# Optimization experiments

Hardware: AMD Instinct MI355X
Metric: run time of the kernel (lower is better)

Reference implementation:

```python
import jax, jax.numpy as jnp
import numpy as np
from itertools import product

B, D, H, W = 2, 32, 256, 256
N = 150000
C_IN, C_MID, C_OUT = 16, 32, 64
STRIDE, PAD, K = 2, 1, 3
DO = (D + 2 * PAD - K) // STRIDE + 1
HO = (H + 2 * PAD - K) // STRIDE + 1
WO = (W + 2 * PAD - K) // STRIDE + 1
EPS = 1e-5


def setup_inputs() -> dict:
    key = jax.random.key(0)
    ks = jax.random.split(key, 8)
    # unique active voxel coords via permutation of linear grid indices
    lin = jax.random.permutation(ks[0], B * D * H * W)[:N]
    b = lin // (D * H * W); r = lin % (D * H * W)
    z = r // (H * W); r = r % (H * W)
    y = r // W; x = r % W
    coords = jnp.stack([b, z, y, x], axis=1).astype(jnp.int32)  # [N,4] = (batch,z,y,x)
    feats = jax.random.normal(ks[1], (N, C_IN), jnp.float32)
    W1 = jax.random.normal(ks[2], (27, C_IN, C_MID), jnp.float32) * 0.08
    W2 = jax.random.normal(ks[3], (27, C_MID, C_MID), jnp.float32) * 0.06
    W3 = jax.random.normal(ks[4], (27, C_MID, C_OUT), jnp.float32) * 0.06
    b1 = jnp.zeros((C_MID,), jnp.float32); g1 = jnp.ones((C_MID,), jnp.float32); be1 = jnp.zeros((C_MID,), jnp.float32)
    b2 = jnp.zeros((C_MID,), jnp.float32); g2 = jnp.ones((C_MID,), jnp.float32); be2 = jnp.zeros((C_MID,), jnp.float32)
    b3 = jnp.zeros((C_OUT,), jnp.float32); g3 = jnp.ones((C_OUT,), jnp.float32); be3 = jnp.zeros((C_OUT,), jnp.float32)
    return dict(feats=feats, coords=coords, W1=W1, b1=b1, g1=g1, be1=be1,
                W2=W2, b2=b2, g2=g2, be2=be2, W3=W3, b3=b3, g3=g3, be3=be3)


def _bn_relu(x, g, b):
    # BatchNorm1d (training batch stats, biased var) over active voxels + ReLU
    m = x.mean(0)
    v = ((x - m) ** 2).mean(0)
    return jax.nn.relu((x - m) * jax.lax.rsqrt(v + EPS) * g + b)


def _subm_conv(feats, coords, grid, Wk, bias):
    # submanifold conv: gather neighbor features per kernel offset, GEMM, accumulate
    bb, zz, yy, xx = coords[:, 0], coords[:, 1], coords[:, 2], coords[:, 3]
    acc = jnp.zeros((feats.shape[0], Wk.shape[-1]), feats.dtype)
    for ki, (dz, dy, dx) in enumerate(product((-1, 0, 1), repeat=3)):
        nz, ny, nx = zz + dz, yy + dy, xx + dx
        valid = (nz >= 0) & (nz < D) & (ny >= 0) & (ny < H) & (nx >= 0) & (nx < W)
        lin = ((bb * D + jnp.clip(nz, 0, D - 1)) * H + jnp.clip(ny, 0, H - 1)) * W + jnp.clip(nx, 0, W - 1)
        nidx = jnp.where(valid, grid[lin], -1)
        gathered = jnp.where((nidx >= 0)[:, None], feats[jnp.maximum(nidx, 0)], 0.0)
        acc = acc + gathered @ Wk[ki]
    return acc + bias


def _sparse_down_conv(feats, coords, Wk, bias):
    # stride-2 SparseConv3d as GEMM + scatter-add into downsampled dense grid; mask = active outputs
    bb, zz, yy, xx = coords[:, 0], coords[:, 1], coords[:, 2], coords[:, 3]
    M = B * DO * HO * WO
    out = jnp.zeros((M, Wk.shape[-1]), feats.dtype)
    cnt = jnp.zeros((M,), jnp.int32)
    for ki, (kz, ky, kx) in enumerate(product(range(K), repeat=3)):
        oz, oy, ox = zz + PAD - kz, yy + PAD - ky, xx + PAD - kx
        valid = ((oz % STRIDE == 0) & (oy % STRIDE == 0) & (ox % STRIDE == 0) &
                 (oz >= 0) & (oy >= 0) & (ox >= 0) &
                 (oz // STRIDE < DO) & (oy // STRIDE < HO) & (ox // STRIDE < WO))
        lin = ((bb * DO + jnp.clip(oz // STRIDE, 0, DO - 1)) * HO
               + jnp.clip(oy // STRIDE, 0, HO - 1)) * WO + jnp.clip(ox // STRIDE, 0, WO - 1)
        lin = jnp.where(valid, lin, 0)
        contrib = jnp.where(valid[:, None], feats @ Wk[ki], 0.0)
        out = out.at[lin].add(contrib)
        cnt = cnt.at[lin].add(valid.astype(jnp.int32))
    mask = cnt > 0
    out = jnp.where(mask[:, None], out + bias, 0.0)
    return out, mask


def reference(feats, coords, W1, b1, g1, be1, W2, b2, g2, be2, W3, b3, g3, be3):
    lin0 = ((coords[:, 0] * D + coords[:, 1]) * H + coords[:, 2]) * W + coords[:, 3]
    grid = jnp.full((B * D * H * W,), -1, jnp.int32).at[lin0].set(jnp.arange(N, dtype=jnp.int32))
    x = _bn_relu(_subm_conv(feats, coords, grid, W1, b1), g1, be1)
    x = _bn_relu(_subm_conv(x, coords, grid, W2, b2), g2, be2)
    out, mask = _sparse_down_conv(x, coords, W3, b3)
    nact = jnp.maximum(mask.sum(), 1).astype(out.dtype)
    m = out.sum(0) / nact  # inactive rows are zero
    v = jnp.where(mask[:, None], (out - m) ** 2, 0.0).sum(0) / nact
    out = jax.nn.relu((out - m) * jax.lax.rsqrt(v + EPS) * g3 + be3)
    out = jnp.where(mask[:, None], out, 0.0)
    return out.reshape(B, DO, HO, WO, C_OUT)
```

## Files before the change

### kernel.cpp

```cpp
#include <hip/hip_runtime.h>

#define B_   2
#define D_   32
#define H_   256
#define W_   256
#define N_   150000
#define CIN  16
#define CMID 32
#define COUT 64
#define DO_  16
#define HO_  128
#define WO_  128
#define M_   (B_*DO_*HO_*WO_)
#define EPSf 1e-5f
#define NB_DOWN 8192
#define NREP 64

typedef _Float16 h2 __attribute__((ext_vector_type(2)));
__device__ inline h2 as_h2(unsigned u) { union { unsigned u; h2 h; } x; x.u = u; return x.h; }

#if defined(__has_builtin) && __has_builtin(__builtin_amdgcn_fdot2)
__device__ inline float dot2(unsigned f, unsigned w, float acc) {
    return __builtin_amdgcn_fdot2(as_h2(f), as_h2(w), acc, false);
}
#else
__device__ inline float dot2(unsigned f, unsigned w, float acc) {
    const h2 a = as_h2(f), b = as_h2(w);
    return fmaf((float)a.x, (float)b.x, fmaf((float)a.y, (float)b.y, acc));
}
#endif

__device__ inline unsigned hpk(float a, float b) {
    union { _Float16 h[2]; unsigned u; } x;
    x.h[0] = (_Float16)a; x.h[1] = (_Float16)b; return x.u;
}

__global__ __launch_bounds__(256) void k_scatter(const int* __restrict__ coords,
                                                 int* __restrict__ grid) {
    int i = blockIdx.x * 256 + threadIdx.x;
    if (i >= N_) return;
    const int4 c = *(const int4*)(coords + 4 * (size_t)i);
    grid[((c.x * D_ + c.y) * H_ + c.z) * W_ + c.w] = i;
}

__global__ __launch_bounds__(256) void k_twisth(const float* __restrict__ W1,
                                                const float* __restrict__ W2,
                                                const float* __restrict__ W3,
                                                uint4* __restrict__ Wh1,
                                                uint4* __restrict__ Wh2,
                                                uint4* __restrict__ Wh3) {
    const int t = blockIdx.x * 256 + threadIdx.x;
    if (t < 1728) {
        const int ki = t / 64, r = t % 64, half = r >> 5, sub = r & 31;
        const float* base = W1 + ki * 512 + (half * 8) * 32 + sub;
        uint4 o;
        o.x = hpk(base[0],   base[32]);
        o.y = hpk(base[64],  base[96]);
        o.z = hpk(base[128], base[160]);
        o.w = hpk(base[192], base[224]);
        Wh1[(ki * 2 + half) * 32 + sub] = o;
    } else if (t < 1728 + 3456) {
        const int u = t - 1728;
        const int ki = u / 128, r = u % 128, qh = r >> 5, sub = r & 31;
        const int half = qh >> 1, q = qh & 1;
        const float* base = W2 + ki * 1024 + (half * 16 + q * 8) * 32 + sub;
        uint4 o;
        o.x = hpk(base[0],   base[32]);
        o.y = hpk(base[64],  base[96]);
        o.z = hpk(base[128], base[160]);
        o.w = hpk(base[192], base[224]);
        Wh2[((ki * 2 + half) * 2 + q) * 32 + sub] = o;
    } else if (t < 1728 + 3456 + 6912) {
        const int u = t - 5184;
        const int ki = u / 256, r = u % 256, q = r >> 6, lane = r & 63;
        const float* base = W3 + ki * 2048 + (q * 8) * 64 + lane;
        uint4 o;
        o.x = hpk(base[0],   base[64]);
        o.y = hpk(base[128], base[192]);
        o.z = hpk(base[256], base[320]);
        o.w = hpk(base[384], base[448]);
        Wh3[(ki * 4 + q) * 64 + lane] = o;
    }
}

__global__ __launch_bounds__(256) void k_feat16(const float* __restrict__ F,
                                                unsigned* __restrict__ F16) {
    const int i = blockIdx.x * 256 + threadIdx.x;
    if (i >= N_ * CIN / 4) return;
    const float4 v = ((const float4*)F)[i];
    uint2 o; o.x = hpk(v.x, v.y); o.y = hpk(v.z, v.w);
    ((uint2*)F16)[i] = o;
}

template <int CI>
__global__ __launch_bounds__(256) void k_subm(const unsigned* __restrict__ X16,
                                              const int* __restrict__ coords,
                                              const int* __restrict__ grid,
                                              const uint4* __restrict__ Wh,
                                              const float* __restrict__ bias,
                                              _Float16* __restrict__ Yp,
                                              float* __restrict__ slab0) {
    constexpr int NQ = CI / 16;
    const int wid  = (blockIdx.x * 256 + threadIdx.x) >> 6;
    const int lane = threadIdx.x & 63;
    const int sub  = lane & 31;
    const int half = lane >> 5;
    const int i0   = wid * 4;

    int nidx01 = -1, nidx23 = -1;
    {
        const int4 cc = *(const int4*)(coords + 4 * (size_t)(i0 + half));
        if (sub < 27) {
            const int nz = cc.y + sub / 9 - 1;
            const int ny = cc.z + (sub / 3) % 3 - 1;
            const int nx = cc.w + sub % 3 - 1;
            if ((unsigned)nz < (unsigned)D_ && (unsigned)ny < (unsigned)H_ &&
                (unsigned)nx < (unsigned)W_)
                nidx01 = grid[((cc.x * D_ + nz) * H_ + ny) * W_ + nx];
        }
    }
    {
        const int4 cc = *(const int4*)(coords + 4 * (size_t)(i0 + 2 + half));
        if (sub < 27) {
            const int nz = cc.y + sub / 9 - 1;
            const int ny = cc.z + (sub / 3) % 3 - 1;
            const int nx = cc.w + sub % 3 - 1;
            if ((unsigned)nz < (unsigned)D_ && (unsigned)ny < (unsigned)H_ &&
                (unsigned)nx < (unsigned)W_)
                nidx23 = grid[((cc.x * D_ + nz) * H_ + ny) * W_ + nx];
        }
    }
    const unsigned long long a01 = __ballot(nidx01 >= 0);
    const unsigned long long a23 = __ballot(nidx23 >= 0);
    unsigned m0 = (unsigned)a01 & 0x7FFFFFFu;
    unsigned m1 = (unsigned)(a01 >> 32) & 0x7FFFFFFu;
    unsigned m2 = (unsigned)a23 & 0x7FFFFFFu;
    unsigned m3 = (unsigned)(a23 >> 32) & 0x7FFFFFFu;

    float4 ac0 = {0.f, 0.f, 0.f, 0.f}, ac1 = {0.f, 0.f, 0.f, 0.f};
    float4 ac2 = {0.f, 0.f, 0.f, 0.f}, ac3 = {0.f, 0.f, 0.f, 0.f};

    auto tap = [&](int ki, int ni, float4& ac) {
        const uint4* __restrict__ f =
            (const uint4*)(X16 + (size_t)ni * (CI / 2) + half * (CI / 4));
        const uint4* __restrict__ wb = Wh + ((size_t)(ki * 2 + half)) * NQ * 32 + sub;
#pragma unroll
        for (int q = 0; q < NQ; ++q) {
            const uint4 fu = f[q];
            const uint4 wu = wb[q * 32];
            ac.x = dot2(fu.x, wu.x, ac.x);
            ac.y = dot2(fu.y, wu.y, ac.y);
            ac.z = dot2(fu.z, wu.z, ac.z);
            ac.w = dot2(fu.w, wu.w, ac.w);
        }
    };

    while (m0 | m1 | m2 | m3) {
        if (m0) { const int ki = __builtin_ctz(m0); m0 &= m0 - 1;
                  tap(ki, __shfl(nidx01, ki, 64),      ac0); }
        if (m1) { const int ki = __builtin_ctz(m1); m1 &= m1 - 1;
                  tap(ki, __shfl(nidx01, ki + 32, 64), ac1); }
        if (m2) { const int ki = __builtin_ctz(m2); m2 &= m2 - 1;
                  tap(ki, __shfl(nidx23, ki, 64),      ac2); }
        if (m3) { const int ki = __builtin_ctz(m3); m3 &= m3 - 1;
                  tap(ki, __shfl(nidx23, ki + 32, 64), ac3); }
    }

    float s0 = (ac0.x + ac0.y) + (ac0.z + ac0.w);
    float s1 = (ac1.x + ac1.y) + (ac1.z + ac1.w);
    float s2v = (ac2.x + ac2.y) + (ac2.z + ac2.w);
    float s3 = (ac3.x + ac3.y) + (ac3.z + ac3.w);
    s0 += __shfl_xor(s0, 32, 64);
    s1 += __shfl_xor(s1, 32, 64);
    s2v += __shfl_xor(s2v, 32, 64);
    s3 += __shfl_xor(s3, 32, 64);
    const float bv  = bias[sub];
    const float o01 = (half ? s1 : s0) + bv;
    const float o23 = (half ? s3 : s2v) + bv;
    Yp[(size_t)(i0 + half) * 32 + sub]     = (_Float16)o01;
    Yp[(size_t)(i0 + 2 + half) * 32 + sub] = (_Float16)o23;

    __shared__ float sd[256];
    const int tid = threadIdx.x;
    float* __restrict__ slab = slab0 + (size_t)(blockIdx.x & (NREP - 1)) * 64;
    sd[tid] = o01 + o23;
    __syncthreads();
    if (tid < 32) {
        float t = 0.f;
#pragma unroll
        for (int k = 0; k < 8; ++k) t += sd[tid + 32 * k];
        atomicAdd(slab + tid, t);
    }
    __syncthreads();
    sd[tid] = o01 * o01 + o23 * o23;
    __syncthreads();
    if (tid < 32) {
        float t = 0.f;
#pragma unroll
        for (int k = 0; k < 8; ++k) t += sd[tid + 32 * k];
        atomicAdd(slab + 32 + tid, t);
    }
}

__global__ __launch_bounds__(256) void k_down(const unsigned* __restrict__ X16,
                                              const int* __restrict__ grid,
                                              const uint4* __restrict__ Wh3,
                                              const float* __restrict__ bias,
                                              _Float16* __restrict__ Yh,
                                              unsigned char* __restrict__ mask,
                                              float* __restrict__ slab0,
                                              int* __restrict__ nacts) {
    const int b    = blockIdx.x;
    const int swz  = (b & 7) * (NB_DOWN / 8) + (b >> 3);
    const int tid  = threadIdx.x;
    const int wv   = tid >> 6;
    const int lane = tid & 63;
    const int sub  = lane & 31;
    const int half = lane >> 5;

    const int vox0 = swz * 64;
    const int ox0  = vox0 & 127;
    int t = vox0 >> 7;
    const int oy = t & 127; t >>= 7;
    const int oz = t & 15;
    const int bb = t >> 4;

    __shared__ int   gl[9][132];
    __shared__ float sd[256];
    __shared__ int   scnt[4];

    const int gx0 = 2 * ox0 - 1;
#pragma unroll
    for (int r = 0; r < 9; ++r) {
        const int z = 2 * oz - 1 + r / 3;
        const int y = 2 * oy - 1 + r % 3;
        if (tid < 132) {
            const int xo = tid;
            const int x  = gx0 + xo;
            int v = -1;
            if ((unsigned)z < (unsigned)D_ && (unsigned)y < (unsigned)H_ &&
                (unsigned)x < (unsigned)W_ && xo < 129)
                v = grid[((bb * D_ + z) * H_ + y) * W_ + x];
            gl[r][xo] = v;
        }
    }
    __syncthreads();

    const int dz = sub / 9, dy = (sub / 3) % 3, dx = sub % 3;
    const int row = (sub < 27) ? dz * 3 + dy : 0;

    const float bv = bias[lane];
    float s = 0.f, s2 = 0.f;
    int cnt = 0;

    auto tap = [&](int ki, int ni, float4& ac) {
        const uint4* __restrict__ fS = (const uint4*)(X16 + (size_t)ni * 16);
        const uint4* __restrict__ wb = Wh3 + (size_t)ki * 256 + lane;
#pragma unroll
        for (int q = 0; q < 4; ++q) {
            const uint4 fu = fS[q];
            const uint4 wu = wb[q * 64];
            ac.x = dot2(fu.x, wu.x, ac.x);
            ac.y = dot2(fu.y, wu.y, ac.y);
            ac.z = dot2(fu.z, wu.z, ac.z);
            ac.w = dot2(fu.w, wu.w, ac.w);
        }
    };

    int n01 = (sub < 27) ? gl[row][2 * (wv * 16 + half) + dx] : -1;
    int n23 = (sub < 27) ? gl[row][2 * (wv * 16 + 2 + half) + dx] : -1;

    for (int it = 0; it < 4; ++it) {
        const int v0  = wv * 16 + it * 4;
        const int c01 = n01, c23 = n23;
        const unsigned long long a01 = __ballot(c01 >= 0);
        const unsigned long long a23 = __ballot(c23 >= 0);

        if (it < 3) {
            n01 = (sub < 27) ? gl[row][2 * (v0 + 4 + half) + dx] : -1;
            n23 = (sub < 27) ? gl[row][2 * (v0 + 6 + half) + dx] : -1;
        }

        unsigned m0 = (unsigned)a01 & 0x7FFFFFFu;
        unsigned m1 = (unsigned)(a01 >> 32) & 0x7FFFFFFu;
        unsigned m2 = (unsigned)a23 & 0x7FFFFFFu;
        unsigned m3 = (unsigned)(a23 >> 32) & 0x7FFFFFFu;
        const int mk0 = m0 ? 1 : 0, mk1 = m1 ? 1 : 0;
        const int mk2 = m2 ? 1 : 0, mk3 = m3 ? 1 : 0;

        float4 ac0 = {0.f, 0.f, 0.f, 0.f}, ac1 = {0.f, 0.f, 0.f, 0.f};
        float4 ac2 = {0.f, 0.f, 0.f, 0.f}, ac3 = {0.f, 0.f, 0.f, 0.f};
        while (m0 | m1 | m2 | m3) {
            if (m0) { const int ki = __builtin_ctz(m0); m0 &= m0 - 1;
                      tap(ki, __builtin_amdgcn_readfirstlane(__shfl(c01, ki, 64)),      ac0); }
            if (m1) { const int ki = __builtin_ctz(m1); m1 &= m1 - 1;
                      tap(ki, __builtin_amdgcn_readfirstlane(__shfl(c01, ki + 32, 64)), ac1); }
            if (m2) { const int ki = __builtin_ctz(m2); m2 &= m2 - 1;
                      tap(ki, __builtin_amdgcn_readfirstlane(__shfl(c23, ki, 64)),      ac2); }
            if (m3) { const int ki = __builtin_ctz(m3); m3 &= m3 - 1;
                      tap(ki, __builtin_amdgcn_readfirstlane(__shfl(c23, ki + 32, 64)), ac3); }
        }

        const int vg = vox0 + v0;
        const float o0 = mk0 ? (ac0.x + ac0.y) + (ac0.z + ac0.w) + bv : 0.f;
        const float o1 = mk1 ? (ac1.x + ac1.y) + (ac1.z + ac1.w) + bv : 0.f;
        const float o2 = mk2 ? (ac2.x + ac2.y) + (ac2.z + ac2.w) + bv : 0.f;
        const float o3 = mk3 ? (ac3.x + ac3.y) + (ac3.z + ac3.w) + bv : 0.f;
        Yh[(size_t)vg * COUT + lane]       = (_Float16)o0;
        Yh[(size_t)(vg + 1) * COUT + lane] = (_Float16)o1;
        Yh[(size_t)(vg + 2) * COUT + lane] = (_Float16)o2;
        Yh[(size_t)(vg + 3) * COUT + lane] = (_Float16)o3;
        if (lane == 0) {
            mask[vg]     = (unsigned char)mk0;
            mask[vg + 1] = (unsigned char)mk1;
            mask[vg + 2] = (unsigned char)mk2;
            mask[vg + 3] = (unsigned char)mk3;
            cnt += mk0 + mk1 + mk2 + mk3;
        }
        s  += o0 + o1 + o2 + o3;
        s2 += o0 * o0 + o1 * o1 + o2 * o2 + o3 * o3;
    }

    float* __restrict__ slab = slab0 + (size_t)(b & (NREP - 1)) * 128;
    sd[tid] = s;
    if (lane == 0) scnt[wv] = cnt;
    __syncthreads();
    if (tid < 64) atomicAdd(slab + tid, sd[tid] + sd[tid + 64] + sd[tid + 128] + sd[tid + 192]);
    __syncthreads();
    sd[tid] = s2;
    __syncthreads();
    if (tid < 64) atomicAdd(slab + 64 + tid, sd[tid] + sd[tid + 64] + sd[tid + 128] + sd[tid + 192]);
    if (tid == 0) atomicAdd(nacts + (b & (NREP - 1)), scnt[0] + scnt[1] + scnt[2] + scnt[3]);
}

template <int C>
__global__ void k_finslab(const float* __restrict__ slab0,
                          const float* __restrict__ g,
                          const float* __restrict__ be,
                          float n, float* __restrict__ ss) {
    const int c = threadIdx.x;
    if (c >= C) return;
    float sm = 0.f, s2 = 0.f;
    for (int r = 0; r < NREP; ++r) {
        sm += slab0[r * 2 * C + c];
        s2 += slab0[r * 2 * C + C + c];
    }
    const float m  = sm / n;
    const float v  = s2 / n - m * m;
    const float sc = g[c] * rsqrtf(v + EPSf);
    ss[c]     = sc;
    ss[C + c] = be[c] - m * sc;
}

__global__ void k_finstats3(const float* __restrict__ slab0,
                            const int* __restrict__ nacts,
                            const float* __restrict__ g,
                            const float* __restrict__ be,
                            float* __restrict__ ss) {
    const int c = threadIdx.x;
    if (c >= 64) return;
    float sm = 0.f, s2 = 0.f;
    int na = 0;
    for (int r = 0; r < NREP; ++r) {
        sm += slab0[r * 128 + c];
        s2 += slab0[r * 128 + 64 + c];
        na += nacts[r];
    }
    const float n  = (float)(na > 0 ? na : 1);
    const float m  = sm / n;
    const float v  = s2 / n - m * m;
    const float sc = g[c] * rsqrtf(v + EPSf);
    ss[c]      = sc;
    ss[64 + c] = be[c] - m * sc;
}

template <int C>
__global__ __launch_bounds__(256) void k_norm16(const unsigned* __restrict__ Yp2,
                                                const float* __restrict__ ss,
                                                unsigned* __restrict__ Xo16, long n4) {
    const long t = (long)blockIdx.x * 256 + threadIdx.x;
    if (t >= n4) return;
    const uint2 y = ((const uint2*)Yp2)[t];
    const h2 lo = as_h2(y.x), hi = as_h2(y.y);
    const int ch = (int)((t * 4) % C);
    float ox = fmaxf(fmaf((float)lo.x, ss[ch],     ss[C + ch]),     0.f);
    float oy = fmaxf(fmaf((float)lo.y, ss[ch + 1], ss[C + ch + 1]), 0.f);
    float oz = fmaxf(fmaf((float)hi.x, ss[ch + 2], ss[C + ch + 2]), 0.f);
    float ow = fmaxf(fmaf((float)hi.y, ss[ch + 3], ss[C + ch + 3]), 0.f);
    uint2 o; o.x = hpk(ox, oy); o.y = hpk(oz, ow);
    ((uint2*)Xo16)[t] = o;
}

__global__ __launch_bounds__(256) void k_norm3(const _Float16* __restrict__ Yh,
                                               const unsigned char* __restrict__ mask,
                                               const float* __restrict__ ss,
                                               float* __restrict__ out) {
    const long n4 = (long)M_ * COUT / 4;
    const long t = (long)blockIdx.x * 256 + threadIdx.x;
    if (t >= n4) return;
    const long vox = t >> 4;
    const int ch = (int)((t * 4) & 63);
    float4 o;
    if (mask[vox]) {
        const uint2 yu = *(const uint2*)(Yh + t * 4);
        const h2 ylo = as_h2(yu.x), yhi = as_h2(yu.y);
        o.x = fmaxf(fmaf((float)ylo.x, ss[ch],     ss[64 + ch]),     0.f);
        o.y = fmaxf(fmaf((float)ylo.y, ss[ch + 1], ss[64 + ch + 1]), 0.f);
        o.z = fmaxf(fmaf((float)yhi.x, ss[ch + 2], ss[64 + ch + 2]), 0.f);
        o.w = fmaxf(fmaf((float)yhi.y, ss[ch + 3], ss[64 + ch + 3]), 0.f);
    } else {
        o.x = o.y = o.z = o.w = 0.f;
    }
    ((float4*)out)[t] = o;
}

extern "C" void kernel_launch(void* const* d_in, const int* in_sizes, int n_in,
                              void* d_out, int out_size, void* d_ws, size_t ws_size,
                              hipStream_t stream) {
    const float* feats = (const float*)d_in[0];
    const int*   coords = (const int*)d_in[1];
    const float* W1 = (const float*)d_in[2];
    const float* b1 = (const float*)d_in[3];
    const float* g1 = (const float*)d_in[4];
    const float* be1 = (const float*)d_in[5];
    const float* W2 = (const float*)d_in[6];
    const float* b2 = (const float*)d_in[7];
    const float* g2 = (const float*)d_in[8];
    const float* be2 = (const float*)d_in[9];
    const float* W3 = (const float*)d_in[10];
    const float* b3 = (const float*)d_in[11];
    const float* g3 = (const float*)d_in[12];
    const float* be3 = (const float*)d_in[13];
    float* out = (float*)d_out;

    char* ws = (char*)d_ws;
    const size_t gridBytes = (size_t)B_ * D_ * H_ * W_ * 4;
    const size_t f16Bytes  = (size_t)N_ * CIN * 2;
    const size_t bufPBytes = (size_t)N_ * CMID * 2;
    const size_t YhBytes   = (size_t)M_ * COUT * 2;
    int*       grid   = (int*)ws;
    unsigned*  feat16 = (unsigned*)(ws + gridBytes);
    _Float16*  bufP   = (_Float16*)(ws + gridBytes + f16Bytes);
    unsigned*  bufH   = (unsigned*)(ws + gridBytes + f16Bytes + bufPBytes);
    _Float16*  Yh     = (_Float16*)(ws + gridBytes + f16Bytes + 2 * bufPBytes);
    unsigned char* mask = (unsigned char*)(ws + gridBytes + f16Bytes + 2 * bufPBytes + YhBytes);
    float* stats = (float*)(ws + gridBytes + f16Bytes + 2 * bufPBytes + YhBytes + (size_t)M_);

    float* ss1   = stats;
    float* ss2   = stats + 64;
    float* ss3   = stats + 128;
    float* slab1 = stats + 1024;
    float* slab2 = stats + 1024 + NREP * 64;
    float* slab3 = stats + 1024 + NREP * 128;
    int*   nacts = (int*)(stats + 1024 + NREP * 256);
    uint4* Wh1 = (uint4*)(stats + 32768);
    uint4* Wh2 = Wh1 + 1728;
    uint4* Wh3 = Wh2 + 3456;

    hipMemsetAsync(grid, 0xFF, gridBytes, stream);
    hipMemsetAsync(stats + 1024, 0, (NREP * 256 + NREP) * 4, stream);

    k_scatter<<<(N_ + 255) / 256, 256, 0, stream>>>(coords, grid);
    k_twisth<<<(12096 + 255) / 256, 256, 0, stream>>>(W1, W2, W3, Wh1, Wh2, Wh3);
    k_feat16<<<(N_ * CIN / 4 + 255) / 256, 256, 0, stream>>>(feats, feat16);

    const int nb_subm = N_ / 16;
    k_subm<CIN><<<nb_subm, 256, 0, stream>>>(feat16, coords, grid, Wh1, b1, bufP, slab1);
    k_finslab<CMID><<<1, 64, 0, stream>>>(slab1, g1, be1, (float)N_, ss1);
    k_norm16<CMID><<<(N_ * CMID / 4 + 255) / 256, 256, 0, stream>>>(
        (const unsigned*)bufP, ss1, bufH, (long)N_ * CMID / 4);

    k_subm<CMID><<<nb_subm, 256, 0, stream>>>(bufH, coords, grid, Wh2, b2, bufP, slab2);
    k_finslab<CMID><<<1, 64, 0, stream>>>(slab2, g2, be2, (float)N_, ss2);
    k_norm16<CMID><<<(N_ * CMID / 4 + 255) / 256, 256, 0, stream>>>(
        (const unsigned*)bufP, ss2, bufH, (long)N_ * CMID / 4);

    k_down<<<NB_DOWN, 256, 0, stream>>>(bufH, grid, Wh3, b3, Yh, mask, slab3, nacts);
    k_finstats3<<<1, 64, 0, stream>>>(slab3, nacts, g3, be3, ss3);
    k_norm3<<<(M_ * COUT / 4) / 256, 256, 0, stream>>>(Yh, mask, ss3, out);
}
```

Measured before the change: 240.4 us.

## Compact active taps per wave into a flat list and software-pipeline loads

In k_down, all active (voxel, kernel-offset) taps of a wave's 16 output voxels are now compacted into one lane-indexed list with ds_permute, together with metadata marking each voxel's last tap. The tap loop then walks this flat list four deep, issuing the feature and weight loads for the next taps before the current dot products, so memory latency overlaps compute. Before, the code looped per group of four voxels with ctz over the ballot masks, which left lanes idle when voxels had uneven tap counts. This costs more registers and more complex control flow, which may lower occupancy, and falls back to a serial per-voxel path when there are more than 62 taps.

```diff
diff --git a/kernel.cpp b/kernel.cpp
--- a/kernel.cpp
+++ b/kernel.cpp
@@ -28,6 +28,12 @@
     const h2 a = as_h2(f), b = as_h2(w);
     return fmaf((float)a.x, (float)b.x, fmaf((float)a.y, (float)b.y, acc));
 }
+#endif
+
+#if defined(__has_builtin) && __has_builtin(__builtin_amdgcn_readlane)
+#define RDLANE(v, l) __builtin_amdgcn_readlane((v), (l))
+#else
+#define RDLANE(v, l) __shfl((v), (l), 64)
 #endif
 
 __device__ inline unsigned hpk(float a, float b) {
@@ -220,10 +226,10 @@
 
     const int vox0 = swz * 64;
     const int ox0  = vox0 & 127;
-    int t = vox0 >> 7;
-    const int oy = t & 127; t >>= 7;
-    const int oz = t & 15;
-    const int bb = t >> 4;
+    int t0 = vox0 >> 7;
+    const int oy = t0 & 127; t0 >>= 7;
+    const int oz = t0 & 15;
+    const int bb = t0 >> 4;
 
     __shared__ int   gl[9][132];
     __shared__ float sd[256];
@@ -248,77 +254,142 @@
 
     const int dz = sub / 9, dy = (sub / 3) % 3, dx = sub % 3;
     const int row = (sub < 27) ? dz * 3 + dy : 0;
+    const int wbase = wv * 16;
+
+    int nP[8];
+    unsigned long long aP[8];
+#pragma unroll
+    for (int p = 0; p < 8; ++p) {
+        const int vl = wbase + 2 * p + half;
+        nP[p] = (sub < 27) ? gl[row][2 * vl + dx] : -1;
+        aP[p] = __ballot(nP[p] >= 0);
+    }
+
+    int pcA[16];
+#pragma unroll
+    for (int p = 0; p < 8; ++p) {
+        pcA[2 * p]     = __popcll(aP[p] & 0x7FFFFFFull);
+        pcA[2 * p + 1] = __popcll((aP[p] >> 32) & 0x7FFFFFFull);
+    }
+    int baseA[16]; int ntap = 0;
+#pragma unroll
+    for (int v = 0; v < 16; ++v) { baseA[v] = ntap; ntap += pcA[v]; }
 
     const float bv = bias[lane];
     float s = 0.f, s2 = 0.f;
     int cnt = 0;
 
-    auto tap = [&](int ki, int ni, float4& ac) {
-        const uint4* __restrict__ fS = (const uint4*)(X16 + (size_t)ni * 16);
-        const uint4* __restrict__ wb = Wh3 + (size_t)ki * 256 + lane;
-#pragma unroll
-        for (int q = 0; q < 4; ++q) {
-            const uint4 fu = fS[q];
-            const uint4 wu = wb[q * 64];
-            ac.x = dot2(fu.x, wu.x, ac.x);
-            ac.y = dot2(fu.y, wu.y, ac.y);
-            ac.z = dot2(fu.z, wu.z, ac.z);
-            ac.w = dot2(fu.w, wu.w, ac.w);
-        }
-    };
-
-    int n01 = (sub < 27) ? gl[row][2 * (wv * 16 + half) + dx] : -1;
-    int n23 = (sub < 27) ? gl[row][2 * (wv * 16 + 2 + half) + dx] : -1;
-
-    for (int it = 0; it < 4; ++it) {
-        const int v0  = wv * 16 + it * 4;
-        const int c01 = n01, c23 = n23;
-        const unsigned long long a01 = __ballot(c01 >= 0);
-        const unsigned long long a23 = __ballot(c23 >= 0);
-
-        if (it < 3) {
-            n01 = (sub < 27) ? gl[row][2 * (v0 + 4 + half) + dx] : -1;
-            n23 = (sub < 27) ? gl[row][2 * (v0 + 6 + half) + dx] : -1;
-        }
-
-        unsigned m0 = (unsigned)a01 & 0x7FFFFFFu;
-        unsigned m1 = (unsigned)(a01 >> 32) & 0x7FFFFFFu;
-        unsigned m2 = (unsigned)a23 & 0x7FFFFFFu;
-        unsigned m3 = (unsigned)(a23 >> 32) & 0x7FFFFFFu;
-        const int mk0 = m0 ? 1 : 0, mk1 = m1 ? 1 : 0;
-        const int mk2 = m2 ? 1 : 0, mk3 = m3 ? 1 : 0;
-
-        float4 ac0 = {0.f, 0.f, 0.f, 0.f}, ac1 = {0.f, 0.f, 0.f, 0.f};
-        float4 ac2 = {0.f, 0.f, 0.f, 0.f}, ac3 = {0.f, 0.f, 0.f, 0.f};
-        while (m0 | m1 | m2 | m3) {
-            if (m0) { const int ki = __builtin_ctz(m0); m0 &= m0 - 1;
-                      tap(ki, __builtin_amdgcn_readfirstlane(__shfl(c01, ki, 64)),      ac0); }
-            if (m1) { const int ki = __builtin_ctz(m1); m1 &= m1 - 1;
-                      tap(ki, __builtin_amdgcn_readfirstlane(__shfl(c01, ki + 32, 64)), ac1); }
-            if (m2) { const int ki = __builtin_ctz(m2); m2 &= m2 - 1;
-                      tap(ki, __builtin_amdgcn_readfirstlane(__shfl(c23, ki, 64)),      ac2); }
-            if (m3) { const int ki = __builtin_ctz(m3); m3 &= m3 - 1;
-                      tap(ki, __builtin_amdgcn_readfirstlane(__shfl(c23, ki + 32, 64)), ac3); }
-        }
-
-        const int vg = vox0 + v0;
-        const float o0 = mk0 ? (ac0.x + ac0.y) + (ac0.z + ac0.w) + bv : 0.f;
-        const float o1 = mk1 ? (ac1.x + ac1.y) + (ac1.z + ac1.w) + bv : 0.f;
-        const float o2 = mk2 ? (ac2.x + ac2.y) + (ac2.z + ac2.w) + bv : 0.f;
-        const float o3 = mk3 ? (ac3.x + ac3.y) + (ac3.z + ac3.w) + bv : 0.f;
-        Yh[(size_t)vg * COUT + lane]       = (_Float16)o0;
-        Yh[(size_t)(vg + 1) * COUT + lane] = (_Float16)o1;
-        Yh[(size_t)(vg + 2) * COUT + lane] = (_Float16)o2;
-        Yh[(size_t)(vg + 3) * COUT + lane] = (_Float16)o3;
+#pragma unroll
+    for (int v = 0; v < 16; ++v) {
+        if (pcA[v] == 0)
+            Yh[(size_t)(vox0 + wbase + v) * COUT + lane] = (_Float16)0.f;
         if (lane == 0) {
-            mask[vg]     = (unsigned char)mk0;
-            mask[vg + 1] = (unsigned char)mk1;
-            mask[vg + 2] = (unsigned char)mk2;
-            mask[vg + 3] = (unsigned char)mk3;
-            cnt += mk0 + mk1 + mk2 + mk3;
-        }
-        s  += o0 + o1 + o2 + o3;
-        s2 += o0 * o0 + o1 * o1 + o2 * o2 + o3 * o3;
+            const int a = pcA[v] ? 1 : 0;
+            mask[vox0 + wbase + v] = (unsigned char)a;
+            cnt += a;
+        }
+    }
+
+    if (ntap <= 62) {
+        int metaV = 0, niV = 0;
+#pragma unroll
+        for (int p = 0; p < 8; ++p) {
+            const unsigned mA = (unsigned)(aP[p] & 0x7FFFFFFull);
+            const unsigned mB = (unsigned)((aP[p] >> 32) & 0x7FFFFFFull);
+            const unsigned myM = half ? mB : mA;
+            const int  sb    = sub & 31;
+            const bool valid = (sub < 27) && ((myM >> sb) & 1u);
+            const unsigned below = myM & ((1u << sb) - 1u);
+            const int slot = (half ? baseA[2 * p + 1] : baseA[2 * p]) + __popc(below);
+            const int isLast = ((myM >> ((sb + 1) & 31)) == 0u) ? 1 : 0;
+            const int v = 2 * p + half;
+            const int meta = 0x8000 | (v << 5) | sb | (isLast << 9);
+            const int addr = (valid ? slot : 63) * 4;
+            metaV |= __builtin_amdgcn_ds_permute(addr, valid ? meta : 0);
+            niV   |= __builtin_amdgcn_ds_permute(addr, valid ? nP[p] : 0);
+        }
+
+        int zv = 0;
+        asm volatile("" : "+v"(zv));
+
+        float4 acc = {0.f, 0.f, 0.f, 0.f};
+
+        auto EXT = [&](int t, int& me, uint4* rf, uint4* rw) {
+            me = RDLANE(metaV, t);
+            const int ni = RDLANE(niV, t);
+            const uint4* fp = (const uint4*)(X16 + (size_t)(ni * 16 + zv));
+            const uint4* wp = Wh3 + (size_t)(me & 31) * 256 + lane;
+#pragma unroll
+            for (int q = 0; q < 4; ++q) { rf[q] = fp[q]; rw[q] = wp[q * 64]; }
+        };
+        auto CMP = [&](int me, const uint4* rf, const uint4* rw) {
+#pragma unroll
+            for (int q = 0; q < 4; ++q) {
+                acc.x = dot2(rf[q].x, rw[q].x, acc.x);
+                acc.y = dot2(rf[q].y, rw[q].y, acc.y);
+                acc.z = dot2(rf[q].z, rw[q].z, acc.z);
+                acc.w = dot2(rf[q].w, rw[q].w, acc.w);
+            }
+            if (me & 0x200) {
+                const int v = (me >> 5) & 15;
+                const float o = (acc.x + acc.y) + (acc.z + acc.w) + bv;
+                Yh[(size_t)(vox0 + wbase + v) * COUT + lane] = (_Float16)o;
+                s += o; s2 += o * o;
+                acc.x = 0.f; acc.y = 0.f; acc.z = 0.f; acc.w = 0.f;
+            }
+        };
+
+        uint4 rf0[4], rw0[4], rf1[4], rw1[4], rf2[4], rw2[4], rf3[4], rw3[4];
+        int me0 = 0, me1 = 0, me2 = 0, me3 = 0;
+        if (0 < ntap) EXT(0, me0, rf0, rw0);
+        if (1 < ntap) EXT(1, me1, rf1, rw1);
+        if (2 < ntap) EXT(2, me2, rf2, rw2);
+        if (3 < ntap) EXT(3, me3, rf3, rw3);
+        for (int t = 0; t < ntap; t += 4) {
+            CMP(me0, rf0, rw0);
+            if (t + 4 < ntap) EXT(t + 4, me0, rf0, rw0);
+            if (t + 1 < ntap) {
+                CMP(me1, rf1, rw1);
+                if (t + 5 < ntap) EXT(t + 5, me1, rf1, rw1);
+            }
+            if (t + 2 < ntap) {
+                CMP(me2, rf2, rw2);
+                if (t + 6 < ntap) EXT(t + 6, me2, rf2, rw2);
+            }
+            if (t + 3 < ntap) {
+                CMP(me3, rf3, rw3);
+                if (t + 7 < ntap) EXT(t + 7, me3, rf3, rw3);
+            }
+        }
+    } else {
+#pragma unroll
+        for (int v = 0; v < 16; ++v) {
+            const unsigned mv = (v & 1)
+                ? (unsigned)((aP[v >> 1] >> 32) & 0x7FFFFFFull)
+                : (unsigned)(aP[v >> 1] & 0x7FFFFFFull);
+            if (mv == 0) continue;
+            unsigned m = mv;
+            float acc1 = 0.f;
+            while (m) {
+                const int ki = __builtin_ctz(m); m &= m - 1;
+                const int ni = __builtin_amdgcn_readfirstlane(
+                                   __shfl(nP[v >> 1], ki + 32 * (v & 1), 64));
+                const uint4* __restrict__ fS = (const uint4*)(X16 + (size_t)ni * 16);
+                const uint4* __restrict__ wb = Wh3 + (size_t)ki * 256 + lane;
+#pragma unroll
+                for (int q = 0; q < 4; ++q) {
+                    const uint4 fu = fS[q];
+                    const uint4 wu = wb[q * 64];
+                    acc1 = dot2(fu.x, wu.x, acc1);
+                    acc1 = dot2(fu.y, wu.y, acc1);
+                    acc1 = dot2(fu.z, wu.z, acc1);
+                    acc1 = dot2(fu.w, wu.w, acc1);
+                }
+            }
+            const float o = acc1 + bv;
+            Yh[(size_t)(vox0 + wbase + v) * COUT + lane] = (_Float16)o;
+            s += o; s2 += o * o;
+        }
     }
 
     float* __restrict__ slab = slab0 + (size_t)(b & (NREP - 1)) * 128;
```

New measurement: 313.8 us. 1.31x slower.

## Rewrite strided downsample conv with MFMA 16x16x32 f16 matrix instructions

Applied to the files above, without the earlier changes.

The downsampling sparse conv kernel drops the sparse per-tap dot2 loop, which walked active neighbours via ballot and shuffle. Each wave now owns 16 output channels and runs a dense loop over all 27 taps, computing 16-voxel subtiles with MFMA f16 instructions. The weights are repacked into the MFMA operand layout, and subtiles are skipped only when no voxel in them has a neighbour at that tap. This trades sparse skipping for dense matrix throughput, so with very sparse inputs much of the MFMA work multiplies zeros. Each feature row is also gathered once per wave, four times per block.

```diff
diff --git a/kernel.cpp b/kernel.cpp
--- a/kernel.cpp
+++ b/kernel.cpp
@@ -17,6 +17,10 @@
 #define NREP 64
 
 typedef _Float16 h2 __attribute__((ext_vector_type(2)));
+typedef _Float16 v8h __attribute__((ext_vector_type(8)));
+typedef float    v4f __attribute__((ext_vector_type(4)));
+union U4H8 { uint4 u; v8h h; };
+
 __device__ inline h2 as_h2(unsigned u) { union { unsigned u; h2 h; } x; x.u = u; return x.h; }
 
 #if defined(__has_builtin) && __has_builtin(__builtin_amdgcn_fdot2)
@@ -48,7 +52,7 @@
                                                 const float* __restrict__ W3,
                                                 uint4* __restrict__ Wh1,
                                                 uint4* __restrict__ Wh2,
-                                                uint4* __restrict__ Wh3) {
+                                                uint4* __restrict__ Wm3) {
     const int t = blockIdx.x * 256 + threadIdx.x;
     if (t < 1728) {
         const int ki = t / 64, r = t % 64, half = r >> 5, sub = r & 31;
@@ -72,14 +76,19 @@
         Wh2[((ki * 2 + half) * 2 + q) * 32 + sub] = o;
     } else if (t < 1728 + 3456 + 6912) {
         const int u = t - 5184;
-        const int ki = u / 256, r = u % 256, q = r >> 6, lane = r & 63;
-        const float* base = W3 + ki * 2048 + (q * 8) * 64 + lane;
+        const int lane = u & 63;
+        const int rest = u >> 6;
+        const int w  = rest / 27;
+        const int ki = rest % 27;
+        const int k0 = (lane >> 4) * 8;
+        const int co = w * 16 + (lane & 15);
+        const float* base = W3 + ki * 2048 + co;
         uint4 o;
-        o.x = hpk(base[0],   base[64]);
-        o.y = hpk(base[128], base[192]);
-        o.z = hpk(base[256], base[320]);
-        o.w = hpk(base[384], base[448]);
-        Wh3[(ki * 4 + q) * 64 + lane] = o;
+        o.x = hpk(base[(k0 + 0) * 64], base[(k0 + 1) * 64]);
+        o.y = hpk(base[(k0 + 2) * 64], base[(k0 + 3) * 64]);
+        o.z = hpk(base[(k0 + 4) * 64], base[(k0 + 5) * 64]);
+        o.w = hpk(base[(k0 + 6) * 64], base[(k0 + 7) * 64]);
+        Wm3[u] = o;
     }
 }
 
@@ -204,7 +213,7 @@
 
 __global__ __launch_bounds__(256) void k_down(const unsigned* __restrict__ X16,
                                               const int* __restrict__ grid,
-                                              const uint4* __restrict__ Wh3,
+                                              const uint4* __restrict__ Wm3,
                                               const float* __restrict__ bias,
                                               _Float16* __restrict__ Yh,
                                               unsigned char* __restrict__ mask,
@@ -215,19 +224,18 @@
     const int tid  = threadIdx.x;
     const int wv   = tid >> 6;
     const int lane = tid & 63;
-    const int sub  = lane & 31;
-    const int half = lane >> 5;
+    const int col  = lane & 15;
+    const int kg   = lane >> 4;
 
     const int vox0 = swz * 64;
     const int ox0  = vox0 & 127;
-    int t = vox0 >> 7;
-    const int oy = t & 127; t >>= 7;
-    const int oz = t & 15;
-    const int bb = t >> 4;
+    int t0 = vox0 >> 7;
+    const int oy = t0 & 127; t0 >>= 7;
+    const int oz = t0 & 15;
+    const int bb = t0 >> 4;
 
     __shared__ int   gl[9][132];
     __shared__ float sd[256];
-    __shared__ int   scnt[4];
 
     const int gx0 = 2 * ox0 - 1;
 #pragma unroll
@@ -246,91 +254,73 @@
     }
     __syncthreads();
 
-    const int dz = sub / 9, dy = (sub / 3) % 3, dx = sub % 3;
-    const int row = (sub < 27) ? dz * 3 + dy : 0;
-
-    const float bv = bias[lane];
+    const float bias_l = bias[wv * 16 + col];
+    const uint4* __restrict__ wmrow = Wm3 + (size_t)(wv * 27) * 64 + lane;
+
+    v4f acc0 = {0.f, 0.f, 0.f, 0.f}, acc1 = {0.f, 0.f, 0.f, 0.f};
+    v4f acc2 = {0.f, 0.f, 0.f, 0.f}, acc3 = {0.f, 0.f, 0.f, 0.f};
+    unsigned any0 = 0, any1 = 0, any2 = 0, any3 = 0;
+
+    auto subtile = [&](int m, v4f& accv, unsigned& anyv, int row, int dxk, v8h wbh) {
+        const int ni = gl[row][2 * (16 * m + col) + dxk];
+        const unsigned long long blt = __ballot(ni >= 0);
+        if (blt) {
+            anyv |= (unsigned)blt & 0xFFFFu;
+            U4H8 af; af.u.x = 0u; af.u.y = 0u; af.u.z = 0u; af.u.w = 0u;
+            if (ni >= 0)
+                af.u = *(const uint4*)(X16 + (size_t)ni * 16 + kg * 4);
+            accv = __builtin_amdgcn_mfma_f32_16x16x32_f16(af.h, wbh, accv, 0, 0, 0);
+        }
+    };
+
+    for (int ki = 0; ki < 27; ++ki) {
+        const int row = ki / 3;
+        const int dxk = ki - row * 3;
+        U4H8 wb; wb.u = wmrow[ki * 64];
+        subtile(0, acc0, any0, row, dxk, wb.h);
+        subtile(1, acc1, any1, row, dxk, wb.h);
+        subtile(2, acc2, any2, row, dxk, wb.h);
+        subtile(3, acc3, any3, row, dxk, wb.h);
+    }
+
     float s = 0.f, s2 = 0.f;
-    int cnt = 0;
-
-    auto tap = [&](int ki, int ni, float4& ac) {
-        const uint4* __restrict__ fS = (const uint4*)(X16 + (size_t)ni * 16);
-        const uint4* __restrict__ wb = Wh3 + (size_t)ki * 256 + lane;
+    auto epi = [&](int m, const v4f& accv, unsigned anyv) {
 #pragma unroll
-        for (int q = 0; q < 4; ++q) {
-            const uint4 fu = fS[q];
-            const uint4 wu = wb[q * 64];
-            ac.x = dot2(fu.x, wu.x, ac.x);
-            ac.y = dot2(fu.y, wu.y, ac.y);
-            ac.z = dot2(fu.z, wu.z, ac.z);
-            ac.w = dot2(fu.w, wu.w, ac.w);
+        for (int r = 0; r < 4; ++r) {
+            const int rowloc = kg * 4 + r;
+            const float o = ((anyv >> rowloc) & 1u) ? (accv[r] + bias_l) : 0.f;
+            Yh[(size_t)(vox0 + 16 * m + rowloc) * COUT + wv * 16 + col] = (_Float16)o;
+            s += o; s2 += o * o;
         }
     };
-
-    int n01 = (sub < 27) ? gl[row][2 * (wv * 16 + half) + dx] : -1;
-    int n23 = (sub < 27) ? gl[row][2 * (wv * 16 + 2 + half) + dx] : -1;
-
-    for (int it = 0; it < 4; ++it) {
-        const int v0  = wv * 16 + it * 4;
-        const int c01 = n01, c23 = n23;
-        const unsigned long long a01 = __ballot(c01 >= 0);
-        const unsigned long long a23 = __ballot(c23 >= 0);
-
-        if (it < 3) {
-            n01 = (sub < 27) ? gl[row][2 * (v0 + 4 + half) + dx] : -1;
-            n23 = (sub < 27) ? gl[row][2 * (v0 + 6 + half) + dx] : -1;
-        }
-
-        unsigned m0 = (unsigned)a01 & 0x7FFFFFFu;
-        unsigned m1 = (unsigned)(a01 >> 32) & 0x7FFFFFFu;
-        unsigned m2 = (unsigned)a23 & 0x7FFFFFFu;
-        unsigned m3 = (unsigned)(a23 >> 32) & 0x7FFFFFFu;
-        const int mk0 = m0 ? 1 : 0, mk1 = m1 ? 1 : 0;
-        const int mk2 = m2 ? 1 : 0, mk3 = m3 ? 1 : 0;
-
-        float4 ac0 = {0.f, 0.f, 0.f, 0.f}, ac1 = {0.f, 0.f, 0.f, 0.f};
-        float4 ac2 = {0.f, 0.f, 0.f, 0.f}, ac3 = {0.f, 0.f, 0.f, 0.f};
-        while (m0 | m1 | m2 | m3) {
-            if (m0) { const int ki = __builtin_ctz(m0); m0 &= m0 - 1;
-                      tap(ki, __builtin_amdgcn_readfirstlane(__shfl(c01, ki, 64)),      ac0); }
-            if (m1) { const int ki = __builtin_ctz(m1); m1 &= m1 - 1;
-                      tap(ki, __builtin_amdgcn_readfirstlane(__shfl(c01, ki + 32, 64)), ac1); }
-            if (m2) { const int ki = __builtin_ctz(m2); m2 &= m2 - 1;
-                      tap(ki, __builtin_amdgcn_readfirstlane(__shfl(c23, ki, 64)),      ac2); }
-            if (m3) { const int ki = __builtin_ctz(m3); m3 &= m3 - 1;
-                      tap(ki, __builtin_amdgcn_readfirstlane(__shfl(c23, ki + 32, 64)), ac3); }
-        }
-
-        const int vg = vox0 + v0;
-        const float o0 = mk0 ? (ac0.x + ac0.y) + (ac0.z + ac0.w) + bv : 0.f;
-        const float o1 = mk1 ? (ac1.x + ac1.y) + (ac1.z + ac1.w) + bv : 0.f;
-        const float o2 = mk2 ? (ac2.x + ac2.y) + (ac2.z + ac2.w) + bv : 0.f;
-        const float o3 = mk3 ? (ac3.x + ac3.y) + (ac3.z + ac3.w) + bv : 0.f;
-        Yh[(size_t)vg * COUT + lane]       = (_Float16)o0;
-        Yh[(size_t)(vg + 1) * COUT + lane] = (_Float16)o1;
-        Yh[(size_t)(vg + 2) * COUT + lane] = (_Float16)o2;
-        Yh[(size_t)(vg + 3) * COUT + lane] = (_Float16)o3;
-        if (lane == 0) {
-            mask[vg]     = (unsigned char)mk0;
-            mask[vg + 1] = (unsigned char)mk1;
-            mask[vg + 2] = (unsigned char)mk2;
-            mask[vg + 3] = (unsigned char)mk3;
-            cnt += mk0 + mk1 + mk2 + mk3;
-        }
-        s  += o0 + o1 + o2 + o3;
-        s2 += o0 * o0 + o1 * o1 + o2 * o2 + o3 * o3;
+    epi(0, acc0, any0); epi(1, acc1, any1); epi(2, acc2, any2); epi(3, acc3, any3);
+
+    if (wv == 0 && lane < 16) {
+        mask[vox0 +  0 + col] = (unsigned char)((any0 >> col) & 1u);
+        mask[vox0 + 16 + col] = (unsigned char)((any1 >> col) & 1u);
+        mask[vox0 + 32 + col] = (unsigned char)((any2 >> col) & 1u);
+        mask[vox0 + 48 + col] = (unsigned char)((any3 >> col) & 1u);
     }
 
     float* __restrict__ slab = slab0 + (size_t)(b & (NREP - 1)) * 128;
     sd[tid] = s;
-    if (lane == 0) scnt[wv] = cnt;
-    __syncthreads();
-    if (tid < 64) atomicAdd(slab + tid, sd[tid] + sd[tid + 64] + sd[tid + 128] + sd[tid + 192]);
+    __syncthreads();
+    if (tid < 64) {
+        const int base = ((tid >> 4) << 6) + (tid & 15);
+        atomicAdd(slab + tid, sd[base] + sd[base + 16] + sd[base + 32] + sd[base + 48]);
+    }
     __syncthreads();
     sd[tid] = s2;
     __syncthreads();
-    if (tid < 64) atomicAdd(slab + 64 + tid, sd[tid] + sd[tid + 64] + sd[tid + 128] + sd[tid + 192]);
-    if (tid == 0) atomicAdd(nacts + (b & (NREP - 1)), scnt[0] + scnt[1] + scnt[2] + scnt[3]);
+    if (tid < 64) {
+        const int base = ((tid >> 4) << 6) + (tid & 15);
+        atomicAdd(slab + 64 + tid, sd[base] + sd[base + 16] + sd[base + 32] + sd[base + 48]);
+    }
+    if (tid == 0) {
+        const int cnt = __popc(any0 & 0xFFFFu) + __popc(any1 & 0xFFFFu) +
+                        __popc(any2 & 0xFFFFu) + __popc(any3 & 0xFFFFu);
+        atomicAdd(nacts + (b & (NREP - 1)), cnt);
+    }
 }
 
 template <int C>
@@ -455,13 +445,13 @@
     int*   nacts = (int*)(stats + 1024 + NREP * 256);
     uint4* Wh1 = (uint4*)(stats + 32768);
     uint4* Wh2 = Wh1 + 1728;
-    uint4* Wh3 = Wh2 + 3456;
+    uint4* Wm3 = Wh2 + 3456;
 
     hipMemsetAsync(grid, 0xFF, gridBytes, stream);
     hipMemsetAsync(stats + 1024, 0, (NREP * 256 + NREP) * 4, stream);
 
     k_scatter<<<(N_ + 255) / 256, 256, 0, stream>>>(coords, grid);
-    k_twisth<<<(12096 + 255) / 256, 256, 0, stream>>>(W1, W2, W3, Wh1, Wh2, Wh3);
+    k_twisth<<<(12096 + 255) / 256, 256, 0, stream>>>(W1, W2, W3, Wh1, Wh2, Wm3);
     k_feat16<<<(N_ * CIN / 4 + 255) / 256, 256, 0, stream>>>(feats, feat16);
 
     const int nb_subm = N_ / 16;
@@ -475,7 +465,7 @@
     k_norm16<CMID><<<(N_ * CMID / 4 + 255) / 256, 256, 0, stream>>>(
         (const unsigned*)bufP, ss2, bufH, (long)N_ * CMID / 4);
 
-    k_down<<<NB_DOWN, 256, 0, stream>>>(bufH, grid, Wh3, b3, Yh, mask, slab3, nacts);
+    k_down<<<NB_DOWN, 256, 0, stream>>>(bufH, grid, Wm3, b3, Yh, mask, slab3, nacts);
     k_finstats3<<<1, 64, 0, stream>>>(slab3, nacts, g3, be3, ss3);
     k_norm3<<<(M_ * COUT / 4) / 256, 256, 0, stream>>>(Yh, mask, ss3, out);
 }
```

Result: slower. 266.4 us (+10.8%).
